# Optimization experiments

Measured on AMD Instinct MI355X. Metric: run time of the kernel, lower is better.

Reference implementation:

```python
import jax, jax.numpy as jnp
import numpy as np

TAU = 0.1
SELF_MASK = 1e6  # added to diagonal of self-distances (y_neg is x)


def _cdist(a, b):
    # pairwise L2 distances, [Na, Nb]; eps keeps sqrt grad finite at 0
    sq = (a * a).sum(-1)[:, None] + (b * b).sum(-1)[None, :] - 2.0 * (a @ b.T)
    return jnp.sqrt(jnp.maximum(sq, 1e-12))


def setup_inputs() -> dict:
    key = jax.random.key(0)
    k1, k2 = jax.random.split(key)
    N, D = 4096, 512
    return {
        "x": jax.random.normal(k1, (N, D), dtype=jnp.float32),
        "y_pos": jax.random.normal(k2, (N, D), dtype=jnp.float32),
    }


def reference(x, y_pos):
    # compute_drift_velocity with y_neg = x (training/loss path)
    N = x.shape[0]
    dist_pos = _cdist(x, y_pos)                      # [N, N]
    dist_neg = _cdist(x, x) + SELF_MASK * jnp.eye(N, dtype=x.dtype)
    logits = -jnp.concatenate([dist_pos, dist_neg], axis=1) / TAU  # [N, 2N]
    # dual normalization: row softmax * column softmax, geometric mean
    A_row = jax.nn.softmax(logits, axis=-1)
    A_col = jax.nn.softmax(logits, axis=0)
    A = jnp.sqrt(A_row * A_col)
    A_pos, A_neg = A[:, :N], A[:, N:]
    drift = A_pos @ y_pos - A_neg @ x                # [N, D]
    return drift
```

## Files before the change

### kernel.cpp

```cpp
#include <hip/hip_runtime.h>
#include <math.h>

#define NN   4096
#define DD   512
#define TWON 8192
#define KSLICE 8

typedef _Float16 half_t;
typedef unsigned short u16;
using half8  = __attribute__((ext_vector_type(8))) half_t;
using short8 = __attribute__((ext_vector_type(8))) short;
using f32x4  = __attribute__((ext_vector_type(4))) float;

__device__ __forceinline__ u16 f2bf(float f) {
    unsigned u = __float_as_uint(f);
    u += 0x7fffu + ((u >> 16) & 1u);
    return (u16)(u >> 16);
}
__device__ __forceinline__ float bf2f(u16 h) {
    return __uint_as_float(((unsigned)h) << 16);
}
__device__ __forceinline__ void gl16(const void* g, void* l) {
    __builtin_amdgcn_global_load_lds(
        (const __attribute__((address_space(1))) void*)g,
        (__attribute__((address_space(3))) void*)l, 16, 0, 0);
}
__device__ __forceinline__ f32x4 mfma16h(half8 a, half8 b, f32x4 c) {
    return __builtin_amdgcn_mfma_f32_16x16x32_f16(a, b, c, 0, 0, 0);
}
__device__ __forceinline__ f32x4 mfma16b(short8 a, short8 b, f32x4 c) {
    return __builtin_amdgcn_mfma_f32_16x16x32_bf16(a, b, c, 0, 0, 0);
}

__global__ __launch_bounds__(64)
void prep_k(const float* __restrict__ x, const float* __restrict__ y,
            half_t* __restrict__ bhi, float* __restrict__ nb) {
    int r = blockIdx.x;
    int l = threadIdx.x;
    const float* src = (r < NN) ? (y + (size_t)r * DD) : (x + (size_t)(r - NN) * DD);
    float4 v0 = *reinterpret_cast<const float4*>(src + l * 8);
    float4 v1 = *reinterpret_cast<const float4*>(src + l * 8 + 4);
    float e[8] = {v0.x, v0.y, v0.z, v0.w, v1.x, v1.y, v1.z, v1.w};
    float s = 0.f;
    half8 h;
    #pragma unroll
    for (int q = 0; q < 8; ++q) {
        s += e[q] * e[q];
        h[q] = (half_t)e[q];
    }
    *reinterpret_cast<half8*>(bhi + (size_t)r * DD + l * 8) = h;
    #pragma unroll
    for (int off = 32; off; off >>= 1) s += __shfl_down(s, off);
    if (l == 0) nb[r] = s;
}

__global__ __launch_bounds__(256)
void b2tr_k(const half_t* __restrict__ bhi, u16* __restrict__ b2t) {
    __shared__ half_t tl[32][33];
    int k0 = blockIdx.x * 32, d0 = blockIdx.y * 32;
    int tx = threadIdx.x, ty = threadIdx.y;
    #pragma unroll
    for (int j = 0; j < 4; ++j)
        tl[ty + 8 * j][tx] = bhi[(size_t)(k0 + ty + 8 * j) * DD + d0 + tx];
    __syncthreads();
    float sgn = (k0 < NN) ? 1.f : -1.f;
    #pragma unroll
    for (int j = 0; j < 4; ++j) {
        float v = (float)tl[tx][ty + 8 * j] * sgn;
        b2t[(size_t)(d0 + ty + 8 * j) * TWON + k0 + tx] = f2bf(v);
    }
}

__global__ __launch_bounds__(256)
void gemm1_k(const half_t* __restrict__ bhi,
             const float* __restrict__ nb, u16* __restrict__ Ef,
             float* __restrict__ Ct,
             float* __restrict__ rpm, float* __restrict__ rps,
             float* __restrict__ cpm, float* __restrict__ cps) {
    __shared__ unsigned char lds[32768];
    const int t = threadIdx.x;
    const int wave = t >> 6, lane = t & 63;
    const int i0 = blockIdx.y * 128, j0 = blockIdx.x * 128;
    const int wm = (wave >> 1) * 64, wn = (wave & 1) * 64;
    const half_t* ahig = bhi + (size_t)NN * DD;
    f32x4 acc[4][4] = {};
    for (int k0 = 0; k0 < DD; k0 += 64) {
        __syncthreads();
        #pragma unroll
        for (int q = 0; q < 4; ++q) {
            const int dbase = (wave * 4 + q) * 1024;
            const int p  = dbase + lane * 16;
            const int r  = p >> 7;
            const int cb = (p & 127) ^ ((r & 7) << 4);
            const size_t offA = (size_t)(i0 + r) * DD + k0 + (cb >> 1);
            const size_t offB = (size_t)(j0 + r) * DD + k0 + (cb >> 1);
            gl16(ahig + offA, lds + dbase);
            gl16(bhi  + offB, lds + 16384 + dbase);
        }
        asm volatile("s_waitcnt vmcnt(0)" ::: "memory");
        __builtin_amdgcn_sched_barrier(0);
        __syncthreads();
        #pragma unroll
        for (int kk = 0; kk < 2; ++kk) {
            half8 ah[4];
            #pragma unroll
            for (int m = 0; m < 4; ++m) {
                const int row = wm + m * 16 + (lane & 15);
                const int off = row * 128 + ((kk * 64 + (lane >> 4) * 16) ^ ((row & 7) << 4));
                ah[m] = *reinterpret_cast<const half8*>(lds + off);
            }
            #pragma unroll
            for (int n = 0; n < 4; ++n) {
                const int row = wn + n * 16 + (lane & 15);
                const int off = row * 128 + ((kk * 64 + (lane >> 4) * 16) ^ ((row & 7) << 4));
                half8 bh = *reinterpret_cast<const half8*>(lds + 16384 + off);
                #pragma unroll
                for (int m = 0; m < 4; ++m)
                    acc[m][n] = mfma16h(ah[m], bh, acc[m][n]);
            }
        }
    }
    float nbj[4];
    #pragma unroll
    for (int n = 0; n < 4; ++n) nbj[n] = nb[j0 + wn + n * 16 + (lane & 15)];
    float tmax = -3.0e38f;
    #pragma unroll
    for (int m = 0; m < 4; ++m) {
        #pragma unroll
        for (int r4 = 0; r4 < 4; ++r4) {
            const int i = i0 + wm + m * 16 + (lane >> 4) * 4 + r4;
            const float nxi = nb[NN + i];
            #pragma unroll
            for (int n = 0; n < 4; ++n) {
                const int j = j0 + wn + n * 16 + (lane & 15);
                float sq = nxi + nbj[n] - 2.0f * acc[m][n][r4];
                float lg = -10.0f * sqrtf(fmaxf(sq, 1e-12f));
                if (j == i + NN) lg = -1e7f;
                acc[m][n][r4] = lg;
                tmax = fmaxf(tmax, lg);
            }
        }
    }
    #pragma unroll
    for (int off = 1; off < 64; off <<= 1) tmax = fmaxf(tmax, __shfl_xor(tmax, off));
    __syncthreads();
    float* red = reinterpret_cast<float*>(lds);
    if (lane == 0) red[wave] = tmax;
    __syncthreads();
    const float C = fmaxf(fmaxf(red[0], red[1]), fmaxf(red[2], red[3]));
    __syncthreads();
    if (t == 0) Ct[blockIdx.y * 64 + blockIdx.x] = C;
    float rs[16] = {}, cs[4] = {};
    #pragma unroll
    for (int m = 0; m < 4; ++m)
        #pragma unroll
        for (int r4 = 0; r4 < 4; ++r4) {
            const int idx = m * 4 + r4;
            const int i = i0 + wm + m * 16 + (lane >> 4) * 4 + r4;
            #pragma unroll
            for (int n = 0; n < 4; ++n) {
                const int j = j0 + wn + n * 16 + (lane & 15);
                float e = __expf(acc[m][n][r4] - C);
                Ef[(size_t)i * TWON + j] = f2bf(e);
                rs[idx] += e;
                cs[n]   += e;
            }
        }
    #pragma unroll
    for (int off = 1; off < 16; off <<= 1) {
        #pragma unroll
        for (int idx = 0; idx < 16; ++idx) rs[idx] += __shfl_xor(rs[idx], off);
    }
    #pragma unroll
    for (int off = 16; off < 64; off <<= 1) {
        #pragma unroll
        for (int n = 0; n < 4; ++n) cs[n] += __shfl_xor(cs[n], off);
    }
    if ((lane & 15) == 0) {
        #pragma unroll
        for (int m = 0; m < 4; ++m)
            #pragma unroll
            for (int r4 = 0; r4 < 4; ++r4) {
                const int r = wm + m * 16 + (lane >> 4) * 4 + r4;
                red[(wave & 1) * 128 + r] = rs[m * 4 + r4];
            }
    }
    if (lane < 16) {
        #pragma unroll
        for (int n = 0; n < 4; ++n) {
            const int c = wn + n * 16 + lane;
            red[256 + (wave >> 1) * 128 + c] = cs[n];
        }
    }
    __syncthreads();
    if (t < 128) {
        float S = red[t] + red[128 + t];
        rpm[(size_t)blockIdx.x * NN + i0 + t] = C;
        rps[(size_t)blockIdx.x * NN + i0 + t] = S;
    } else {
        const int c = t - 128;
        float S = red[256 + c] + red[384 + c];
        cpm[(size_t)blockIdx.y * TWON + j0 + c] = C;
        cps[(size_t)blockIdx.y * TWON + j0 + c] = S;
    }
}

__global__ __launch_bounds__(256)
void row_comb_k(const float* __restrict__ rpm, const float* __restrict__ rps,
                float* __restrict__ rm, float* __restrict__ rrs) {
    int i = blockIdx.x * 256 + threadIdx.x;
    float M = -3.0e38f;
    for (int tt = 0; tt < TWON / 128; ++tt) M = fmaxf(M, rpm[(size_t)tt * NN + i]);
    float S = 0.f;
    for (int tt = 0; tt < TWON / 128; ++tt)
        S += rps[(size_t)tt * NN + i] * __expf(rpm[(size_t)tt * NN + i] - M);
    rm[i] = M; rrs[i] = rsqrtf(S);
}

__global__ __launch_bounds__(256)
void col_comb_k(const float* __restrict__ cpm, const float* __restrict__ cps,
                float* __restrict__ Pj) {
    int j = blockIdx.x * 256 + threadIdx.x;
    float M = -3.0e38f;
    for (int tt = 0; tt < NN / 128; ++tt) M = fmaxf(M, cpm[(size_t)tt * TWON + j]);
    float S = 0.f;
    for (int tt = 0; tt < NN / 128; ++tt)
        S += cps[(size_t)tt * TWON + j] * __expf(cpm[(size_t)tt * TWON + j] - M);
    Pj[j] = -0.5f * M - 0.5f * logf(S);
}

__global__ __launch_bounds__(512, 4)
void gemm2_k(const u16* __restrict__ Ef, const u16* __restrict__ b2t,
             const float* __restrict__ Ct, const float* __restrict__ rm,
             const float* __restrict__ Pj, const float* __restrict__ rrs,
             unsigned* __restrict__ part) {
    __shared__ unsigned char lds[16384];
    const int t = threadIdx.x;
    const int wave = t >> 6, lane = t & 63;
    const int sw = blockIdx.x;
    const int kslice = sw & 7;
    const int i0 = (sw >> 3) * 64;
    const int ib = (sw >> 3) >> 1;
    const int kbase = kslice * (TWON / KSLICE);
    const int wn = wave * 64;
    const int sr = t >> 3;
    const int kc = (t & 7) * 8;
    const int awbyte = sr * 128 + ((kc * 2) ^ ((sr & 7) << 4));
    const int NT = (TWON / KSLICE) / 64;
    const float rmh = 0.5f * rm[i0 + sr];
    f32x4 acc[4][4] = {};
    short8 aE;
    float4 p0, p1;
    float arg;
    auto LOADA = [&](int it) {
        const int k = kbase + it * 64 + kc;
        aE = *reinterpret_cast<const short8*>(Ef + (size_t)(i0 + sr) * TWON + k);
        p0 = *reinterpret_cast<const float4*>(Pj + k);
        p1 = *reinterpret_cast<const float4*>(Pj + k + 4);
        arg = Ct[ib * 64 + ((kbase + it * 64) >> 7)] - rmh;
    };
    auto STOREA = [&](int buf) {
        short8 g;
        g[0] = (short)f2bf(bf2f((u16)aE[0]) * __expf(arg + p0.x));
        g[1] = (short)f2bf(bf2f((u16)aE[1]) * __expf(arg + p0.y));
        g[2] = (short)f2bf(bf2f((u16)aE[2]) * __expf(arg + p0.z));
        g[3] = (short)f2bf(bf2f((u16)aE[3]) * __expf(arg + p0.w));
        g[4] = (short)f2bf(bf2f((u16)aE[4]) * __expf(arg + p1.x));
        g[5] = (short)f2bf(bf2f((u16)aE[5]) * __expf(arg + p1.y));
        g[6] = (short)f2bf(bf2f((u16)aE[6]) * __expf(arg + p1.z));
        g[7] = (short)f2bf(bf2f((u16)aE[7]) * __expf(arg + p1.w));
        *reinterpret_cast<short8*>(lds + buf * 8192 + awbyte) = g;
    };
    LOADA(0);
    STOREA(0);
    __syncthreads();
    int cur = 0;
    for (int it = 0; it < NT; ++it) {
        short8 bfr0[4], bfr1[4];
        #pragma unroll
        for (int n = 0; n < 4; ++n) {
            const int d = wn + n * 16 + (lane & 15);
            const u16* bp = b2t + (size_t)d * TWON + kbase + it * 64 + (lane >> 4) * 8;
            bfr0[n] = *reinterpret_cast<const short8*>(bp);
            bfr1[n] = *reinterpret_cast<const short8*>(bp + 32);
        }
        if (it + 1 < NT) LOADA(it + 1);
        #pragma unroll
        for (int kk = 0; kk < 2; ++kk) {
            short8 af[4];
            #pragma unroll
            for (int m = 0; m < 4; ++m) {
                const int row = m * 16 + (lane & 15);
                const int off = cur * 8192 + row * 128 +
                                ((kk * 64 + (lane >> 4) * 16) ^ ((row & 7) << 4));
                af[m] = *reinterpret_cast<const short8*>(lds + off);
            }
            #pragma unroll
            for (int m = 0; m < 4; ++m)
                #pragma unroll
                for (int n = 0; n < 4; ++n)
                    acc[m][n] = mfma16b(af[m], (kk == 0) ? bfr0[n] : bfr1[n], acc[m][n]);
        }
        if (it + 1 < NT) STOREA(cur ^ 1);
        __syncthreads();
        cur ^= 1;
    }
    unsigned* pout = part + ((size_t)(kslice * 64 + (sw >> 3)) * 512 + t) * 32;
    #pragma unroll
    for (int m = 0; m < 4; ++m) {
        float rf[4];
        #pragma unroll
        for (int r4 = 0; r4 < 4; ++r4) rf[r4] = rrs[i0 + m * 16 + (lane >> 4) * 4 + r4];
        unsigned pk[8];
        #pragma unroll
        for (int n = 0; n < 4; ++n) {
            pk[n * 2]     = (unsigned)f2bf(acc[m][n][0] * rf[0]) |
                            ((unsigned)f2bf(acc[m][n][1] * rf[1]) << 16);
            pk[n * 2 + 1] = (unsigned)f2bf(acc[m][n][2] * rf[2]) |
                            ((unsigned)f2bf(acc[m][n][3] * rf[3]) << 16);
        }
        *reinterpret_cast<uint4*>(pout + m * 8)     = *reinterpret_cast<uint4*>(pk);
        *reinterpret_cast<uint4*>(pout + m * 8 + 4) = *reinterpret_cast<uint4*>(pk + 4);
    }
}

__global__ __launch_bounds__(512)
void reduce_k(const unsigned* __restrict__ part, float* __restrict__ out) {
    const int b = blockIdx.x;
    const int iblk = b >> 2, mq = b & 3;
    const int t = threadIdx.x;
    const int lane = t & 63, wave = t >> 6;
    float s[16] = {};
    #pragma unroll
    for (int ks = 0; ks < KSLICE; ++ks) {
        const unsigned* p = part + ((size_t)(ks * 64 + iblk) * 512 + t) * 32 + mq * 8;
        uint4 a = *reinterpret_cast<const uint4*>(p);
        uint4 c = *reinterpret_cast<const uint4*>(p + 4);
        unsigned u[8] = {a.x, a.y, a.z, a.w, c.x, c.y, c.z, c.w};
        #pragma unroll
        for (int n = 0; n < 4; ++n) {
            s[n * 4 + 0] += bf2f((u16)(u[n * 2] & 0xffffu));
            s[n * 4 + 1] += bf2f((u16)(u[n * 2] >> 16));
            s[n * 4 + 2] += bf2f((u16)(u[n * 2 + 1] & 0xffffu));
            s[n * 4 + 3] += bf2f((u16)(u[n * 2 + 1] >> 16));
        }
    }
    #pragma unroll
    for (int n = 0; n < 4; ++n)
        #pragma unroll
        for (int r4 = 0; r4 < 4; ++r4) {
            const int i = iblk * 64 + mq * 16 + (lane >> 4) * 4 + r4;
            const int d = wave * 64 + n * 16 + (lane & 15);
            out[(size_t)i * DD + d] = s[n * 4 + r4];
        }
}

extern "C" void kernel_launch(void* const* d_in, const int* in_sizes, int n_in,
                              void* d_out, int out_size, void* d_ws, size_t ws_size,
                              hipStream_t stream) {
    const float* x = (const float*)d_in[0];
    const float* y = (const float*)d_in[1];
    float* out = (float*)d_out;

    char* w = (char*)d_ws;
    const size_t OFF_EF   = 0;
    const size_t OFF_BHI  = 67108864;
    const size_t OFF_B2T  = OFF_BHI + 8388608;
    const size_t OFF_PART = OFF_B2T + 8388608;
    const size_t OFF_RPM  = OFF_PART + 67108864;
    const size_t OFF_RPS  = OFF_RPM + 1048576;
    const size_t OFF_CPM  = OFF_RPS + 1048576;
    const size_t OFF_CPS  = OFF_CPM + 1048576;
    const size_t OFF_CT   = OFF_CPS + 1048576;
    const size_t OFF_TAIL = OFF_CT + 65536;

    u16*      Ef   = (u16*)(w + OFF_EF);
    half_t*   bhi  = (half_t*)(w + OFF_BHI);
    u16*      b2t  = (u16*)(w + OFF_B2T);
    unsigned* part = (unsigned*)(w + OFF_PART);
    float*    rpm  = (float*)(w + OFF_RPM);
    float*    rps  = (float*)(w + OFF_RPS);
    float*    cpm  = (float*)(w + OFF_CPM);
    float*    cps  = (float*)(w + OFF_CPS);
    float*    Ct   = (float*)(w + OFF_CT);
    float*    nb   = (float*)(w + OFF_TAIL);
    float*    rm   = nb  + TWON;
    float*    rrs  = rm  + NN;
    float*    Pj   = rrs + NN;

    prep_k<<<TWON, 64, 0, stream>>>(x, y, bhi, nb);
    gemm1_k<<<dim3(TWON / 128, NN / 128), 256, 0, stream>>>(bhi, nb, Ef, Ct,
                                                            rpm, rps, cpm, cps);
    row_comb_k<<<NN / 256, 256, 0, stream>>>(rpm, rps, rm, rrs);
    col_comb_k<<<TWON / 256, 256, 0, stream>>>(cpm, cps, Pj);
    b2tr_k<<<dim3(TWON / 32, DD / 32), dim3(32, 8), 0, stream>>>(bhi, b2t);
    gemm2_k<<<512, 512, 0, stream>>>(Ef, b2t, Ct, rm, Pj, rrs, part);
    reduce_k<<<256, 512, 0, stream>>>(part, out);
}
```

Measured before the change: 200.5 us.

## Retile gemm2 to 128x256 blocks with four K-slices

```diff
diff --git a/kernel.cpp b/kernel.cpp
--- a/kernel.cpp
+++ b/kernel.cpp
@@ -4,7 +4,6 @@
 #define NN   4096
 #define DD   512
 #define TWON 8192
-#define KSLICE 8
 
 typedef _Float16 half_t;
 typedef unsigned short u16;
@@ -229,47 +228,63 @@
     Pj[j] = -0.5f * M - 0.5f * logf(S);
 }
 
-__global__ __launch_bounds__(512, 4)
+__global__ __launch_bounds__(512, 2)
 void gemm2_k(const u16* __restrict__ Ef, const u16* __restrict__ b2t,
              const float* __restrict__ Ct, const float* __restrict__ rm,
              const float* __restrict__ Pj, const float* __restrict__ rrs,
              unsigned* __restrict__ part) {
-    __shared__ unsigned char lds[16384];
+    __shared__ unsigned char lds[32768];
     const int t = threadIdx.x;
     const int wave = t >> 6, lane = t & 63;
     const int sw = blockIdx.x;
-    const int kslice = sw & 7;
-    const int i0 = (sw >> 3) * 64;
-    const int ib = (sw >> 3) >> 1;
-    const int kbase = kslice * (TWON / KSLICE);
-    const int wn = wave * 64;
+    const int kslice = sw & 3;
+    const int db = (sw >> 2) & 1;
+    const int iblk = sw >> 3;
+    const int i0 = iblk * 128;
+    const int d0 = db * 256;
+    const int kbase = kslice * 2048;
+    const int mh = wave >> 2, dq = wave & 3;
     const int sr = t >> 3;
     const int kc = (t & 7) * 8;
-    const int awbyte = sr * 128 + ((kc * 2) ^ ((sr & 7) << 4));
-    const int NT = (TWON / KSLICE) / 64;
-    const float rmh = 0.5f * rm[i0 + sr];
+    const int awb = sr * 128 + ((kc * 2) ^ ((sr & 7) << 4));
+    const int NT = 32;
+    const float rmh0 = 0.5f * rm[i0 + sr];
+    const float rmh1 = 0.5f * rm[i0 + 64 + sr];
     f32x4 acc[4][4] = {};
-    short8 aE;
+    short8 aE0, aE1;
     float4 p0, p1;
-    float arg;
+    float arg0, arg1;
     auto LOADA = [&](int it) {
         const int k = kbase + it * 64 + kc;
-        aE = *reinterpret_cast<const short8*>(Ef + (size_t)(i0 + sr) * TWON + k);
+        aE0 = *reinterpret_cast<const short8*>(Ef + (size_t)(i0 + sr) * TWON + k);
+        aE1 = *reinterpret_cast<const short8*>(Ef + (size_t)(i0 + 64 + sr) * TWON + k);
         p0 = *reinterpret_cast<const float4*>(Pj + k);
         p1 = *reinterpret_cast<const float4*>(Pj + k + 4);
-        arg = Ct[ib * 64 + ((kbase + it * 64) >> 7)] - rmh;
+        const float ct = Ct[iblk * 64 + ((kbase + it * 64) >> 7)];
+        arg0 = ct - rmh0;
+        arg1 = ct - rmh1;
     };
     auto STOREA = [&](int buf) {
         short8 g;
-        g[0] = (short)f2bf(bf2f((u16)aE[0]) * __expf(arg + p0.x));
-        g[1] = (short)f2bf(bf2f((u16)aE[1]) * __expf(arg + p0.y));
-        g[2] = (short)f2bf(bf2f((u16)aE[2]) * __expf(arg + p0.z));
-        g[3] = (short)f2bf(bf2f((u16)aE[3]) * __expf(arg + p0.w));
-        g[4] = (short)f2bf(bf2f((u16)aE[4]) * __expf(arg + p1.x));
-        g[5] = (short)f2bf(bf2f((u16)aE[5]) * __expf(arg + p1.y));
-        g[6] = (short)f2bf(bf2f((u16)aE[6]) * __expf(arg + p1.z));
-        g[7] = (short)f2bf(bf2f((u16)aE[7]) * __expf(arg + p1.w));
-        *reinterpret_cast<short8*>(lds + buf * 8192 + awbyte) = g;
+        g[0] = (short)f2bf(bf2f((u16)aE0[0]) * __expf(arg0 + p0.x));
+        g[1] = (short)f2bf(bf2f((u16)aE0[1]) * __expf(arg0 + p0.y));
+        g[2] = (short)f2bf(bf2f((u16)aE0[2]) * __expf(arg0 + p0.z));
+        g[3] = (short)f2bf(bf2f((u16)aE0[3]) * __expf(arg0 + p0.w));
+        g[4] = (short)f2bf(bf2f((u16)aE0[4]) * __expf(arg0 + p1.x));
+        g[5] = (short)f2bf(bf2f((u16)aE0[5]) * __expf(arg0 + p1.y));
+        g[6] = (short)f2bf(bf2f((u16)aE0[6]) * __expf(arg0 + p1.z));
+        g[7] = (short)f2bf(bf2f((u16)aE0[7]) * __expf(arg0 + p1.w));
+        *reinterpret_cast<short8*>(lds + buf * 16384 + awb) = g;
+        short8 h;
+        h[0] = (short)f2bf(bf2f((u16)aE1[0]) * __expf(arg1 + p0.x));
+        h[1] = (short)f2bf(bf2f((u16)aE1[1]) * __expf(arg1 + p0.y));
+        h[2] = (short)f2bf(bf2f((u16)aE1[2]) * __expf(arg1 + p0.z));
+        h[3] = (short)f2bf(bf2f((u16)aE1[3]) * __expf(arg1 + p0.w));
+        h[4] = (short)f2bf(bf2f((u16)aE1[4]) * __expf(arg1 + p1.x));
+        h[5] = (short)f2bf(bf2f((u16)aE1[5]) * __expf(arg1 + p1.y));
+        h[6] = (short)f2bf(bf2f((u16)aE1[6]) * __expf(arg1 + p1.z));
+        h[7] = (short)f2bf(bf2f((u16)aE1[7]) * __expf(arg1 + p1.w));
+        *reinterpret_cast<short8*>(lds + buf * 16384 + 8192 + awb) = h;
     };
     LOADA(0);
     STOREA(0);
@@ -279,7 +294,7 @@
         short8 bfr0[4], bfr1[4];
         #pragma unroll
         for (int n = 0; n < 4; ++n) {
-            const int d = wn + n * 16 + (lane & 15);
+            const int d = d0 + dq * 64 + n * 16 + (lane & 15);
             const u16* bp = b2t + (size_t)d * TWON + kbase + it * 64 + (lane >> 4) * 8;
             bfr0[n] = *reinterpret_cast<const short8*>(bp);
             bfr1[n] = *reinterpret_cast<const short8*>(bp + 32);
@@ -290,8 +305,8 @@
             short8 af[4];
             #pragma unroll
             for (int m = 0; m < 4; ++m) {
-                const int row = m * 16 + (lane & 15);
-                const int off = cur * 8192 + row * 128 +
+                const int row = mh * 64 + m * 16 + (lane & 15);
+                const int off = cur * 16384 + row * 128 +
                                 ((kk * 64 + (lane >> 4) * 16) ^ ((row & 7) << 4));
                 af[m] = *reinterpret_cast<const short8*>(lds + off);
             }
@@ -305,12 +320,13 @@
         __syncthreads();
         cur ^= 1;
     }
-    unsigned* pout = part + ((size_t)(kslice * 64 + (sw >> 3)) * 512 + t) * 32;
+    unsigned* pout = part + ((size_t)(kslice * 64 + iblk * 2 + db) * 512 + t) * 32;
     #pragma unroll
     for (int m = 0; m < 4; ++m) {
         float rf[4];
         #pragma unroll
-        for (int r4 = 0; r4 < 4; ++r4) rf[r4] = rrs[i0 + m * 16 + (lane >> 4) * 4 + r4];
+        for (int r4 = 0; r4 < 4; ++r4)
+            rf[r4] = rrs[i0 + mh * 64 + m * 16 + (lane >> 4) * 4 + r4];
         unsigned pk[8];
         #pragma unroll
         for (int n = 0; n < 4; ++n) {
@@ -327,13 +343,14 @@
 __global__ __launch_bounds__(512)
 void reduce_k(const unsigned* __restrict__ part, float* __restrict__ out) {
     const int b = blockIdx.x;
-    const int iblk = b >> 2, mq = b & 3;
+    const int mq = b & 3, db = (b >> 2) & 1, iblk = b >> 3;
     const int t = threadIdx.x;
     const int lane = t & 63, wave = t >> 6;
+    const int mh = wave >> 2, dq = wave & 3;
     float s[16] = {};
     #pragma unroll
-    for (int ks = 0; ks < KSLICE; ++ks) {
-        const unsigned* p = part + ((size_t)(ks * 64 + iblk) * 512 + t) * 32 + mq * 8;
+    for (int ks = 0; ks < 4; ++ks) {
+        const unsigned* p = part + ((size_t)(ks * 64 + iblk * 2 + db) * 512 + t) * 32 + mq * 8;
         uint4 a = *reinterpret_cast<const uint4*>(p);
         uint4 c = *reinterpret_cast<const uint4*>(p + 4);
         unsigned u[8] = {a.x, a.y, a.z, a.w, c.x, c.y, c.z, c.w};
@@ -349,8 +366,8 @@
     for (int n = 0; n < 4; ++n)
         #pragma unroll
         for (int r4 = 0; r4 < 4; ++r4) {
-            const int i = iblk * 64 + mq * 16 + (lane >> 4) * 4 + r4;
-            const int d = wave * 64 + n * 16 + (lane & 15);
+            const int i = iblk * 128 + mh * 64 + mq * 16 + (lane >> 4) * 4 + r4;
+            const int d = db * 256 + dq * 64 + n * 16 + (lane & 15);
             out[(size_t)i * DD + d] = s[n * 4 + r4];
         }
 }
@@ -394,6 +411,6 @@
     row_comb_k<<<NN / 256, 256, 0, stream>>>(rpm, rps, rm, rrs);
     col_comb_k<<<TWON / 256, 256, 0, stream>>>(cpm, cps, Pj);
     b2tr_k<<<dim3(TWON / 32, DD / 32), dim3(32, 8), 0, stream>>>(bhi, b2t);
-    gemm2_k<<<512, 512, 0, stream>>>(Ef, b2t, Ct, rm, Pj, rrs, part);
+    gemm2_k<<<256, 512, 0, stream>>>(Ef, b2t, Ct, rm, Pj, rrs, part);
     reduce_k<<<256, 512, 0, stream>>>(part, out);
 }
```

Result: slower. 212.2 us (+5.9%).

## Retile gemm2 into 128x128 output tiles with B staged in LDS via direct loads

Applied to the files above, without the earlier changes.

```diff
diff --git a/kernel.cpp b/kernel.cpp
--- a/kernel.cpp
+++ b/kernel.cpp
@@ -4,7 +4,6 @@
 #define NN   4096
 #define DD   512
 #define TWON 8192
-#define KSLICE 8
 
 typedef _Float16 half_t;
 typedef unsigned short u16;
@@ -234,111 +233,128 @@
              const float* __restrict__ Ct, const float* __restrict__ rm,
              const float* __restrict__ Pj, const float* __restrict__ rrs,
              unsigned* __restrict__ part) {
-    __shared__ unsigned char lds[16384];
+    __shared__ unsigned char lds[32768];
     const int t = threadIdx.x;
     const int wave = t >> 6, lane = t & 63;
     const int sw = blockIdx.x;
     const int kslice = sw & 7;
-    const int i0 = (sw >> 3) * 64;
-    const int ib = (sw >> 3) >> 1;
-    const int kbase = kslice * (TWON / KSLICE);
-    const int wn = wave * 64;
-    const int sr = t >> 3;
-    const int kc = (t & 7) * 8;
-    const int awbyte = sr * 128 + ((kc * 2) ^ ((sr & 7) << 4));
-    const int NT = (TWON / KSLICE) / 64;
+    const int idx2 = sw >> 3;
+    const int db = idx2 & 3;
+    const int iblk = idx2 >> 2;
+    const int i0 = iblk * 128;
+    const int d0 = db * 128;
+    const int kbase = kslice * 1024;
+    const int mh = wave >> 2, dq = wave & 3;
+    const int sr = t >> 2;
+    const int kc = (t & 3) * 16;
+    const int aw0 = sr * 128 + ((kc * 2) ^ ((sr & 7) << 4));
+    const int aw1 = sr * 128 + (((kc + 8) * 2) ^ ((sr & 7) << 4));
     const float rmh = 0.5f * rm[i0 + sr];
-    f32x4 acc[4][4] = {};
-    short8 aE;
-    float4 p0, p1;
-    float arg;
-    auto LOADA = [&](int it) {
-        const int k = kbase + it * 64 + kc;
-        aE = *reinterpret_cast<const short8*>(Ef + (size_t)(i0 + sr) * TWON + k);
-        p0 = *reinterpret_cast<const float4*>(Pj + k);
-        p1 = *reinterpret_cast<const float4*>(Pj + k + 4);
-        arg = Ct[ib * 64 + ((kbase + it * 64) >> 7)] - rmh;
-    };
-    auto STOREA = [&](int buf) {
-        short8 g;
-        g[0] = (short)f2bf(bf2f((u16)aE[0]) * __expf(arg + p0.x));
-        g[1] = (short)f2bf(bf2f((u16)aE[1]) * __expf(arg + p0.y));
-        g[2] = (short)f2bf(bf2f((u16)aE[2]) * __expf(arg + p0.z));
-        g[3] = (short)f2bf(bf2f((u16)aE[3]) * __expf(arg + p0.w));
-        g[4] = (short)f2bf(bf2f((u16)aE[4]) * __expf(arg + p1.x));
-        g[5] = (short)f2bf(bf2f((u16)aE[5]) * __expf(arg + p1.y));
-        g[6] = (short)f2bf(bf2f((u16)aE[6]) * __expf(arg + p1.z));
-        g[7] = (short)f2bf(bf2f((u16)aE[7]) * __expf(arg + p1.w));
-        *reinterpret_cast<short8*>(lds + buf * 8192 + awbyte) = g;
-    };
-    LOADA(0);
-    STOREA(0);
-    __syncthreads();
-    int cur = 0;
+    const int NT = 16;
+    f32x4 acc[4][2] = {};
     for (int it = 0; it < NT; ++it) {
-        short8 bfr0[4], bfr1[4];
-        #pragma unroll
-        for (int n = 0; n < 4; ++n) {
-            const int d = wn + n * 16 + (lane & 15);
-            const u16* bp = b2t + (size_t)d * TWON + kbase + it * 64 + (lane >> 4) * 8;
-            bfr0[n] = *reinterpret_cast<const short8*>(bp);
-            bfr1[n] = *reinterpret_cast<const short8*>(bp + 32);
-        }
-        if (it + 1 < NT) LOADA(it + 1);
+        __syncthreads();
+        #pragma unroll
+        for (int q = 0; q < 2; ++q) {
+            const int dbase = (wave * 2 + q) * 1024;
+            const int p  = dbase + lane * 16;
+            const int r  = p >> 7;
+            const int cb = (p & 127) ^ ((r & 7) << 4);
+            gl16(b2t + (size_t)(d0 + r) * TWON + kbase + it * 64 + (cb >> 1),
+                 lds + 16384 + dbase);
+        }
+        {
+            const int k = kbase + it * 64 + kc;
+            const u16* ep = Ef + (size_t)(i0 + sr) * TWON + k;
+            short8 aE0 = *reinterpret_cast<const short8*>(ep);
+            short8 aE1 = *reinterpret_cast<const short8*>(ep + 8);
+            float4 p0 = *reinterpret_cast<const float4*>(Pj + k);
+            float4 p1 = *reinterpret_cast<const float4*>(Pj + k + 4);
+            float4 p2 = *reinterpret_cast<const float4*>(Pj + k + 8);
+            float4 p3 = *reinterpret_cast<const float4*>(Pj + k + 12);
+            const float arg = Ct[iblk * 64 + ((kbase + it * 64) >> 7)] - rmh;
+            short8 g0, g1;
+            g0[0] = (short)f2bf(bf2f((u16)aE0[0]) * __expf(arg + p0.x));
+            g0[1] = (short)f2bf(bf2f((u16)aE0[1]) * __expf(arg + p0.y));
+            g0[2] = (short)f2bf(bf2f((u16)aE0[2]) * __expf(arg + p0.z));
+            g0[3] = (short)f2bf(bf2f((u16)aE0[3]) * __expf(arg + p0.w));
+            g0[4] = (short)f2bf(bf2f((u16)aE0[4]) * __expf(arg + p1.x));
+            g0[5] = (short)f2bf(bf2f((u16)aE0[5]) * __expf(arg + p1.y));
+            g0[6] = (short)f2bf(bf2f((u16)aE0[6]) * __expf(arg + p1.z));
+            g0[7] = (short)f2bf(bf2f((u16)aE0[7]) * __expf(arg + p1.w));
+            g1[0] = (short)f2bf(bf2f((u16)aE1[0]) * __expf(arg + p2.x));
+            g1[1] = (short)f2bf(bf2f((u16)aE1[1]) * __expf(arg + p2.y));
+            g1[2] = (short)f2bf(bf2f((u16)aE1[2]) * __expf(arg + p2.z));
+            g1[3] = (short)f2bf(bf2f((u16)aE1[3]) * __expf(arg + p2.w));
+            g1[4] = (short)f2bf(bf2f((u16)aE1[4]) * __expf(arg + p3.x));
+            g1[5] = (short)f2bf(bf2f((u16)aE1[5]) * __expf(arg + p3.y));
+            g1[6] = (short)f2bf(bf2f((u16)aE1[6]) * __expf(arg + p3.z));
+            g1[7] = (short)f2bf(bf2f((u16)aE1[7]) * __expf(arg + p3.w));
+            *reinterpret_cast<short8*>(lds + aw0) = g0;
+            *reinterpret_cast<short8*>(lds + aw1) = g1;
+        }
+        asm volatile("s_waitcnt vmcnt(0)" ::: "memory");
+        __builtin_amdgcn_sched_barrier(0);
+        __syncthreads();
         #pragma unroll
         for (int kk = 0; kk < 2; ++kk) {
-            short8 af[4];
+            short8 af[4], bfr[2];
             #pragma unroll
             for (int m = 0; m < 4; ++m) {
-                const int row = m * 16 + (lane & 15);
-                const int off = cur * 8192 + row * 128 +
+                const int row = mh * 64 + m * 16 + (lane & 15);
+                const int off = row * 128 +
                                 ((kk * 64 + (lane >> 4) * 16) ^ ((row & 7) << 4));
                 af[m] = *reinterpret_cast<const short8*>(lds + off);
             }
             #pragma unroll
+            for (int n = 0; n < 2; ++n) {
+                const int row = dq * 32 + n * 16 + (lane & 15);
+                const int off = 16384 + row * 128 +
+                                ((kk * 64 + (lane >> 4) * 16) ^ ((row & 7) << 4));
+                bfr[n] = *reinterpret_cast<const short8*>(lds + off);
+            }
+            #pragma unroll
             for (int m = 0; m < 4; ++m)
                 #pragma unroll
-                for (int n = 0; n < 4; ++n)
-                    acc[m][n] = mfma16b(af[m], (kk == 0) ? bfr0[n] : bfr1[n], acc[m][n]);
-        }
-        if (it + 1 < NT) STOREA(cur ^ 1);
-        __syncthreads();
-        cur ^= 1;
-    }
-    unsigned* pout = part + ((size_t)(kslice * 64 + (sw >> 3)) * 512 + t) * 32;
+                for (int n = 0; n < 2; ++n)
+                    acc[m][n] = mfma16b(af[m], bfr[n], acc[m][n]);
+        }
+    }
+    unsigned* pout = part + ((size_t)(kslice * 128 + idx2) * 512 + t) * 16;
     #pragma unroll
     for (int m = 0; m < 4; ++m) {
         float rf[4];
         #pragma unroll
-        for (int r4 = 0; r4 < 4; ++r4) rf[r4] = rrs[i0 + m * 16 + (lane >> 4) * 4 + r4];
-        unsigned pk[8];
-        #pragma unroll
-        for (int n = 0; n < 4; ++n) {
+        for (int r4 = 0; r4 < 4; ++r4)
+            rf[r4] = rrs[i0 + mh * 64 + m * 16 + (lane >> 4) * 4 + r4];
+        unsigned pk[4];
+        #pragma unroll
+        for (int n = 0; n < 2; ++n) {
             pk[n * 2]     = (unsigned)f2bf(acc[m][n][0] * rf[0]) |
                             ((unsigned)f2bf(acc[m][n][1] * rf[1]) << 16);
             pk[n * 2 + 1] = (unsigned)f2bf(acc[m][n][2] * rf[2]) |
                             ((unsigned)f2bf(acc[m][n][3] * rf[3]) << 16);
         }
-        *reinterpret_cast<uint4*>(pout + m * 8)     = *reinterpret_cast<uint4*>(pk);
-        *reinterpret_cast<uint4*>(pout + m * 8 + 4) = *reinterpret_cast<uint4*>(pk + 4);
+        *reinterpret_cast<uint4*>(pout + m * 4) = *reinterpret_cast<uint4*>(pk);
     }
 }
 
 __global__ __launch_bounds__(512)
 void reduce_k(const unsigned* __restrict__ part, float* __restrict__ out) {
     const int b = blockIdx.x;
-    const int iblk = b >> 2, mq = b & 3;
+    const int mq = b & 3, pos = b >> 2;
+    const int db = pos & 3, iblk = pos >> 2;
     const int t = threadIdx.x;
     const int lane = t & 63, wave = t >> 6;
-    float s[16] = {};
-    #pragma unroll
-    for (int ks = 0; ks < KSLICE; ++ks) {
-        const unsigned* p = part + ((size_t)(ks * 64 + iblk) * 512 + t) * 32 + mq * 8;
+    const int mh = wave >> 2, dq = wave & 3;
+    float s[8] = {};
+    #pragma unroll
+    for (int ks = 0; ks < 8; ++ks) {
+        const unsigned* p = part + ((size_t)(ks * 128 + pos) * 512 + t) * 16 + mq * 4;
         uint4 a = *reinterpret_cast<const uint4*>(p);
-        uint4 c = *reinterpret_cast<const uint4*>(p + 4);
-        unsigned u[8] = {a.x, a.y, a.z, a.w, c.x, c.y, c.z, c.w};
-        #pragma unroll
-        for (int n = 0; n < 4; ++n) {
+        unsigned u[4] = {a.x, a.y, a.z, a.w};
+        #pragma unroll
+        for (int n = 0; n < 2; ++n) {
             s[n * 4 + 0] += bf2f((u16)(u[n * 2] & 0xffffu));
             s[n * 4 + 1] += bf2f((u16)(u[n * 2] >> 16));
             s[n * 4 + 2] += bf2f((u16)(u[n * 2 + 1] & 0xffffu));
@@ -346,11 +362,11 @@
         }
     }
     #pragma unroll
-    for (int n = 0; n < 4; ++n)
+    for (int n = 0; n < 2; ++n)
         #pragma unroll
         for (int r4 = 0; r4 < 4; ++r4) {
-            const int i = iblk * 64 + mq * 16 + (lane >> 4) * 4 + r4;
-            const int d = wave * 64 + n * 16 + (lane & 15);
+            const int i = iblk * 128 + mh * 64 + mq * 16 + (lane >> 4) * 4 + r4;
+            const int d = db * 128 + dq * 32 + n * 16 + (lane & 15);
             out[(size_t)i * DD + d] = s[n * 4 + r4];
         }
 }
@@ -394,6 +410,6 @@
     row_comb_k<<<NN / 256, 256, 0, stream>>>(rpm, rps, rm, rrs);
     col_comb_k<<<TWON / 256, 256, 0, stream>>>(cpm, cps, Pj);
     b2tr_k<<<dim3(TWON / 32, DD / 32), dim3(32, 8), 0, stream>>>(bhi, b2t);
-    gemm2_k<<<512, 512, 0, stream>>>(Ef, b2t, Ct, rm, Pj, rrs, part);
-    reduce_k<<<256, 512, 0, stream>>>(part, out);
-}
+    gemm2_k<<<1024, 512, 0, stream>>>(Ef, b2t, Ct, rm, Pj, rrs, part);
+    reduce_k<<<512, 512, 0, stream>>>(part, out);
+}
```

New measurement: 187.4 us. 1.07x faster.
